# Kernel tuning notes

Hardware: AMD Instinct MI355X
Metric: run time of the kernel (lower is better)

## Reference

```python
import jax, jax.numpy as jnp
import numpy as np

SHIFT = 1  # torch module picks +/-1 randomly at init; fixed to +1 here


def setup_inputs() -> dict:
    key = jax.random.key(0)
    kx, kw = jax.random.split(key)
    x = jax.random.normal(kx, (128, 24, 112, 112), dtype=jnp.float32)
    w = jax.random.normal(kw, (12, 12, 7), dtype=jnp.float32)  # (in_j, out_i, k)
    return {"x": x, "w": w}


def reference(x, w):
    # The unfold+einsum in the original is a grouped (groups=2) 1D conv over the
    # width axis, kernel size 7, padding 3, with the SAME (12,12,7) weight for
    # both groups. einsum 'lojnkm,jik->loinm' contracts in-channel j and tap k.
    k = jnp.transpose(w, (1, 0, 2))          # (out=12, in=12, 7)
    k = jnp.concatenate([k, k], axis=0)      # (24, 12, 7): group0 then group1
    k = k[:, :, None, :]                     # OIHW: (24, 12, 1, 7)
    y = jax.lax.conv_general_dilated(
        x, k,
        window_strides=(1, 1),
        padding=[(0, 0), (3, 3)],            # conv only along width (last axis)
        dimension_numbers=("NCHW", "OIHW", "NCHW"),
        feature_group_count=2,
    )                                        # (128, 24, 112, 112)
    return jnp.roll(y, SHIFT, axis=2)        # roll along height axis
```

## Files before the change

kernel.cpp:

```cpp
#include <hip/hip_runtime.h>


#define HW 112
#define CHSTRIDE (112 * 112)
#define QPR 28

__global__ __launch_bounds__(256) void conv1x7_grouped_roll(
    const float* __restrict__ x,
    const float* __restrict__ wgt,
    float* __restrict__ out)
{
    int qid = blockIdx.x * 256 + threadIdx.x;
    int w0q = qid % QPR;
    int tmp = qid / QPR;
    int h   = tmp % HW;
    tmp    /= HW;
    int g   = tmp & 1;
    int n   = tmp >> 1;
    int w0  = w0q * 4;

    const float* xbase = x + ((size_t)(n * 24 + g * 12) * HW + h) * HW;

    float acc[12][4];
    #pragma unroll
    for (int o = 0; o < 12; ++o)
        #pragma unroll
        for (int p = 0; p < 4; ++p) acc[o][p] = 0.f;

    bool ok[10];
    int  idx[10];
    #pragma unroll
    for (int t = 0; t < 10; ++t) {
        int wi = w0 - 3 + t;
        ok[t]  = (unsigned)wi < (unsigned)HW;
        idx[t] = ok[t] ? wi : 0;
    }

    for (int ic = 0; ic < 12; ++ic) {
        const float* xr = xbase + (size_t)ic * CHSTRIDE;
        float xv[10];
        #pragma unroll
        for (int t = 0; t < 10; ++t) {
            float v = xr[idx[t]];
            xv[t] = ok[t] ? v : 0.f;
        }
        const float* wr = wgt + ic * 84;
        #pragma unroll
        for (int o = 0; o < 12; ++o) {
            #pragma unroll
            for (int t = 0; t < 7; ++t) {
                float wv = wr[o * 7 + t];
                #pragma unroll
                for (int p = 0; p < 4; ++p)
                    acc[o][p] = fmaf(xv[t + p], wv, acc[o][p]);
            }
        }
    }

    int ho = h + 1; if (ho >= HW) ho = 0;
    float* ob = out + ((size_t)(n * 24 + g * 12) * HW + ho) * HW + w0;
    #pragma unroll
    for (int o = 0; o < 12; ++o) {
        float4 v = make_float4(acc[o][0], acc[o][1], acc[o][2], acc[o][3]);
        *reinterpret_cast<float4*>(ob + (size_t)o * CHSTRIDE) = v;
    }
}

extern "C" void kernel_launch(void* const* d_in, const int* in_sizes, int n_in,
                              void* d_out, int out_size, void* d_ws, size_t ws_size,
                              hipStream_t stream)
{
    const float* x = (const float*)d_in[0];
    const float* w = (const float*)d_in[1];
    float* out = (float*)d_out;

    dim3 grid(3136), block(256);
    hipLaunchKernelGGL(conv1x7_grouped_roll, grid, block, 0, stream, x, w, out);
}
```

Measured before the change: 310.3 us.

## Stage input row and weights in LDS and split output channels across threads

Each block now loads one (n,h) row for all 24 channels into shared memory with vectorized loads and zero padding, and stages the weights there too. Threads read shifted windows from LDS instead of redundant scalar global loads. Each thread computes 3 output channels × 4 pixels instead of 12 × 4, which cuts register pressure and raises occupancy at the cost of some idle lanes and per-block weight reloads.

```diff
diff --git a/kernel.cpp b/kernel.cpp
--- a/kernel.cpp
+++ b/kernel.cpp
@@ -1,68 +1,92 @@
 #include <hip/hip_runtime.h>
 
 
-#define HW 112
-#define CHSTRIDE (112 * 112)
-#define QPR 28
+#define CHS 12544
+#define ROWP 120
 
-__global__ __launch_bounds__(256) void conv1x7_grouped_roll(
+__global__ __launch_bounds__(256, 8) void conv1x7_lds(
     const float* __restrict__ x,
     const float* __restrict__ wgt,
     float* __restrict__ out)
 {
-    int qid = blockIdx.x * 256 + threadIdx.x;
-    int w0q = qid % QPR;
-    int tmp = qid / QPR;
-    int h   = tmp % HW;
-    tmp    /= HW;
-    int g   = tmp & 1;
-    int n   = tmp >> 1;
-    int w0  = w0q * 4;
+    __shared__ float xs[24 * ROWP];
+    __shared__ float ws[12 * 12 * 8];
 
-    const float* xbase = x + ((size_t)(n * 24 + g * 12) * HW + h) * HW;
+    const int b   = blockIdx.x;
+    const int n   = b / 112;
+    const int h   = b % 112;
+    const int tid = threadIdx.x;
 
-    float acc[12][4];
+    const float* xrow = x + (size_t)n * 24 * CHS + h * 112;
     #pragma unroll
-    for (int o = 0; o < 12; ++o)
+    for (int j0 = 0; j0 < 3; ++j0) {
+        int j = j0 * 256 + tid;
+        if (j < 672) {
+            int c  = j / 28;
+            int wq = j % 28;
+            float4 v = *reinterpret_cast<const float4*>(xrow + (size_t)c * CHS + wq * 4);
+            *reinterpret_cast<float4*>(&xs[c * ROWP + 4 + wq * 4]) = v;
+        }
+    }
+    if (tid < 48) {
+        int c   = tid >> 1;
+        int off = (tid & 1) ? 116 : 0;
+        *reinterpret_cast<float4*>(&xs[c * ROWP + off]) = make_float4(0.f, 0.f, 0.f, 0.f);
+    }
+    #pragma unroll
+    for (int j0 = 0; j0 < 4; ++j0) {
+        int j = j0 * 256 + tid;
+        if (j < 1008) {
+            int ic = j / 84, r = j % 84;
+            int oc = r / 7,  t = r % 7;
+            ws[ic * 96 + oc * 8 + t] = wgt[j];
+        }
+    }
+    __syncthreads();
+
+    const int ocset = tid >> 5;
+    const int q     = tid & 31;
+    const int g     = ocset >> 2;
+    const int oc0   = ocset * 3;
+    const int ocl0  = oc0 - g * 12;
+
+    if (q < 28) {
+        float acc[3][4];
         #pragma unroll
-        for (int p = 0; p < 4; ++p) acc[o][p] = 0.f;
+        for (int j = 0; j < 3; ++j)
+            #pragma unroll
+            for (int p = 0; p < 4; ++p) acc[j][p] = 0.f;
 
-    bool ok[10];
-    int  idx[10];
-    #pragma unroll
-    for (int t = 0; t < 10; ++t) {
-        int wi = w0 - 3 + t;
-        ok[t]  = (unsigned)wi < (unsigned)HW;
-        idx[t] = ok[t] ? wi : 0;
-    }
-
-    for (int ic = 0; ic < 12; ++ic) {
-        const float* xr = xbase + (size_t)ic * CHSTRIDE;
-        float xv[10];
         #pragma unroll
-        for (int t = 0; t < 10; ++t) {
-            float v = xr[idx[t]];
-            xv[t] = ok[t] ? v : 0.f;
-        }
-        const float* wr = wgt + ic * 84;
-        #pragma unroll
-        for (int o = 0; o < 12; ++o) {
+        for (int ic = 0; ic < 12; ++ic) {
+            const float* xr = &xs[(g * 12 + ic) * ROWP + 4 * q];
+            float4 xa = *reinterpret_cast<const float4*>(xr);
+            float4 xb = *reinterpret_cast<const float4*>(xr + 4);
+            float4 xc = *reinterpret_cast<const float4*>(xr + 8);
+            float xv[12] = {xa.x, xa.y, xa.z, xa.w,
+                            xb.x, xb.y, xb.z, xb.w,
+                            xc.x, xc.y, xc.z, xc.w};
             #pragma unroll
-            for (int t = 0; t < 7; ++t) {
-                float wv = wr[o * 7 + t];
+            for (int j = 0; j < 3; ++j) {
+                const float* wr = &ws[ic * 96 + (ocl0 + j) * 8];
+                float4 wa = *reinterpret_cast<const float4*>(wr);
+                float4 wb = *reinterpret_cast<const float4*>(wr + 4);
+                float wv[7] = {wa.x, wa.y, wa.z, wa.w, wb.x, wb.y, wb.z};
                 #pragma unroll
-                for (int p = 0; p < 4; ++p)
-                    acc[o][p] = fmaf(xv[t + p], wv, acc[o][p]);
+                for (int t = 0; t < 7; ++t)
+                    #pragma unroll
+                    for (int p = 0; p < 4; ++p)
+                        acc[j][p] = fmaf(xv[1 + t + p], wv[t], acc[j][p]);
             }
         }
-    }
 
-    int ho = h + 1; if (ho >= HW) ho = 0;
-    float* ob = out + ((size_t)(n * 24 + g * 12) * HW + ho) * HW + w0;
-    #pragma unroll
-    for (int o = 0; o < 12; ++o) {
-        float4 v = make_float4(acc[o][0], acc[o][1], acc[o][2], acc[o][3]);
-        *reinterpret_cast<float4*>(ob + (size_t)o * CHSTRIDE) = v;
+        int ho = h + 1; if (ho == 112) ho = 0;
+        float* ob = out + (size_t)(n * 24 + oc0) * CHS + ho * 112 + 4 * q;
+        #pragma unroll
+        for (int j = 0; j < 3; ++j) {
+            *reinterpret_cast<float4*>(ob + (size_t)j * CHS) =
+                make_float4(acc[j][0], acc[j][1], acc[j][2], acc[j][3]);
+        }
     }
 }
 
@@ -74,6 +98,6 @@
     const float* w = (const float*)d_in[1];
     float* out = (float*)d_out;
 
-    dim3 grid(3136), block(256);
-    hipLaunchKernelGGL(conv1x7_grouped_roll, grid, block, 0, stream, x, w, out);
+    dim3 grid(128 * 112), block(256);
+    hipLaunchKernelGGL(conv1x7_lds, grid, block, 0, stream, x, w, out);
 }
```

Measured after the change: 353.3 us. +13.8%, slower.

## Vectorize input loads and transpose weights for float4 weight fetches

Applied to the files above, without the earlier changes.

Adds a small pre-kernel that transposes the weights into (ic, tap, oc) order so each tap's twelve output-channel weights load as three float4s. The main kernel replaces ten scalar bounds-checked input loads per channel with three aligned float4 loads plus edge zeroing. It also remaps threads so a 448-thread block covers eight full rows across both groups. The aim is fewer load instructions and less address arithmetic, at the cost of an extra kernel launch and a workspace buffer.

```diff
diff --git a/kernel.cpp b/kernel.cpp
--- a/kernel.cpp
+++ b/kernel.cpp
@@ -1,69 +1,77 @@
 #include <hip/hip_runtime.h>
 
 
-#define HW 112
-#define CHSTRIDE (112 * 112)
-#define QPR 28
+#define CHS 12544
 
-__global__ __launch_bounds__(256) void conv1x7_grouped_roll(
+__global__ void prep_w(const float* __restrict__ wgt, float* __restrict__ wT) {
+    int j = blockIdx.x * 256 + threadIdx.x;
+    if (j < 1008) {
+        int ic = j / 84, r = j % 84;
+        int oc = r / 7,  t = r % 7;
+        wT[(ic * 7 + t) * 12 + oc] = wgt[j];
+    }
+}
+
+__global__ __launch_bounds__(448) void conv1x7_reg(
     const float* __restrict__ x,
-    const float* __restrict__ wgt,
+    const float* __restrict__ wT,
     float* __restrict__ out)
 {
-    int qid = blockIdx.x * 256 + threadIdx.x;
-    int w0q = qid % QPR;
-    int tmp = qid / QPR;
-    int h   = tmp % HW;
-    tmp    /= HW;
-    int g   = tmp & 1;
-    int n   = tmp >> 1;
-    int w0  = w0q * 4;
+    const int t448  = threadIdx.x;
+    const int rowid = blockIdx.x * 8 + t448 / 56;
+    const int l56   = t448 % 56;
+    const int n = rowid / 112;
+    const int h = rowid % 112;
+    const int g = l56 / 28;
+    const int q = l56 % 28;
+    const int w0 = q * 4;
 
-    const float* xbase = x + ((size_t)(n * 24 + g * 12) * HW + h) * HW;
+    const float* xrow = x + ((size_t)(n * 24 + g * 12) * 112 + h) * 112;
+
+    const bool q0  = (q == 0);
+    const bool q27 = (q == 27);
+    const int offA = q0  ? 0   : (w0 - 4);
+    const int offC = q27 ? 108 : (w0 + 4);
 
     float acc[12][4];
     #pragma unroll
     for (int o = 0; o < 12; ++o)
+        acc[o][0] = acc[o][1] = acc[o][2] = acc[o][3] = 0.f;
+
+    #pragma unroll 2
+    for (int ic = 0; ic < 12; ++ic) {
+        const float* xr = xrow + (size_t)ic * CHS;
+        float4 xa = *reinterpret_cast<const float4*>(xr + offA);
+        float4 xb = *reinterpret_cast<const float4*>(xr + w0);
+        float4 xc = *reinterpret_cast<const float4*>(xr + offC);
+        if (q0)  xa = make_float4(0.f, 0.f, 0.f, 0.f);
+        if (q27) xc = make_float4(0.f, 0.f, 0.f, 0.f);
+        const float xv[12] = {xa.x, xa.y, xa.z, xa.w,
+                              xb.x, xb.y, xb.z, xb.w,
+                              xc.x, xc.y, xc.z, xc.w};
+        const float* wr = wT + ic * 84;
         #pragma unroll
-        for (int p = 0; p < 4; ++p) acc[o][p] = 0.f;
-
-    bool ok[10];
-    int  idx[10];
-    #pragma unroll
-    for (int t = 0; t < 10; ++t) {
-        int wi = w0 - 3 + t;
-        ok[t]  = (unsigned)wi < (unsigned)HW;
-        idx[t] = ok[t] ? wi : 0;
-    }
-
-    for (int ic = 0; ic < 12; ++ic) {
-        const float* xr = xbase + (size_t)ic * CHSTRIDE;
-        float xv[10];
-        #pragma unroll
-        for (int t = 0; t < 10; ++t) {
-            float v = xr[idx[t]];
-            xv[t] = ok[t] ? v : 0.f;
-        }
-        const float* wr = wgt + ic * 84;
-        #pragma unroll
-        for (int o = 0; o < 12; ++o) {
+        for (int t = 0; t < 7; ++t) {
+            float4 wA = *reinterpret_cast<const float4*>(wr + t * 12);
+            float4 wB = *reinterpret_cast<const float4*>(wr + t * 12 + 4);
+            float4 wC = *reinterpret_cast<const float4*>(wr + t * 12 + 8);
+            const float wv[12] = {wA.x, wA.y, wA.z, wA.w,
+                                  wB.x, wB.y, wB.z, wB.w,
+                                  wC.x, wC.y, wC.z, wC.w};
             #pragma unroll
-            for (int t = 0; t < 7; ++t) {
-                float wv = wr[o * 7 + t];
+            for (int o = 0; o < 12; ++o)
                 #pragma unroll
                 for (int p = 0; p < 4; ++p)
-                    acc[o][p] = fmaf(xv[t + p], wv, acc[o][p]);
-            }
+                    acc[o][p] = fmaf(xv[1 + t + p], wv[o], acc[o][p]);
         }
     }
 
-    int ho = h + 1; if (ho >= HW) ho = 0;
-    float* ob = out + ((size_t)(n * 24 + g * 12) * HW + ho) * HW + w0;
+    int ho = h + 1; if (ho == 112) ho = 0;
+    float* ob = out + ((size_t)(n * 24 + g * 12) * 112 + ho) * 112 + w0;
     #pragma unroll
-    for (int o = 0; o < 12; ++o) {
-        float4 v = make_float4(acc[o][0], acc[o][1], acc[o][2], acc[o][3]);
-        *reinterpret_cast<float4*>(ob + (size_t)o * CHSTRIDE) = v;
-    }
+    for (int o = 0; o < 12; ++o)
+        *reinterpret_cast<float4*>(ob + (size_t)o * CHS) =
+            make_float4(acc[o][0], acc[o][1], acc[o][2], acc[o][3]);
 }
 
 extern "C" void kernel_launch(void* const* d_in, const int* in_sizes, int n_in,
@@ -73,7 +81,8 @@
     const float* x = (const float*)d_in[0];
     const float* w = (const float*)d_in[1];
     float* out = (float*)d_out;
+    float* wT  = (float*)d_ws;
 
-    dim3 grid(3136), block(256);
-    hipLaunchKernelGGL(conv1x7_grouped_roll, grid, block, 0, stream, x, w, out);
+    hipLaunchKernelGGL(prep_w, dim3(4), dim3(256), 0, stream, w, wT);
+    hipLaunchKernelGGL(conv1x7_reg, dim3(1792), dim3(448), 0, stream, x, wT, out);
 }
```

After: 290.9 us. 6.3% less time.
